# Kernel tuning notes

Measured on AMD Instinct MI355X. Metric: run time of the kernel, lower is better.

Reference implementation:

```python
import jax, jax.numpy as jnp
import numpy as np

POS_HALF = 4   # positive window: [t-4, t+4)
NEG_LEN = 12   # negatives: up to 12 frames on each side of the positive window
K_MAX = 2 * POS_HALF + 2 * NEG_LEN  # 32 candidates max per timestep


def _build_windows(T):
    """Static [T,K_MAX] gather indices + positive/valid masks (numpy, trace-time)."""
    idx = np.zeros((T, K_MAX), np.int32)
    pos_mask = np.zeros((T, K_MAX), bool)
    valid = np.zeros((T, K_MAX), bool)
    for t in range(T):
        start, end = max(0, t - POS_HALF), min(T, t + POS_HALF)
        pos = list(range(start, end))
        neg = list(range(max(0, start - NEG_LEN), start)) + \
              list(range(end, min(T, end + NEG_LEN)))
        comb = pos + neg
        idx[t, :len(comb)] = comb
        valid[t, :len(comb)] = True
        pos_mask[t, :len(pos)] = True
    return jnp.asarray(idx), jnp.asarray(pos_mask), jnp.asarray(valid)


def _directional(q, kv, idx, pos_mask, valid, scale, bias):
    # q, kv: [B,T,D] (L2-normalized); idx/pos_mask/valid: [T,K]
    w = kv[:, idx]  # [B,T,K,D] windowed gather
    logits = jnp.einsum('btd,btkd->btk', q, w) * scale + bias  # [B,T,K]
    sign = jnp.where(pos_mask, 1.0, -1.0)
    loglik = jax.nn.log_sigmoid(sign * logits)
    # per-t: sum over window, mean over batch; then sum over t
    loss = -jnp.where(valid, loglik, 0.0).sum(axis=2).mean(axis=0).sum()
    am = jnp.argmax(jnp.where(valid, logits, -jnp.inf), axis=2)  # [B,T]
    T = q.shape[1]
    correct = pos_mask[jnp.arange(T)[None, :], am].astype(jnp.float32).sum()
    return loss, correct


def setup_inputs() -> dict:
    key = jax.random.key(0)
    k1, k2 = jax.random.split(key)
    B, T, D = 8, 1024, 512
    return {
        "motion_feature": jax.random.normal(k1, (B, T, D), jnp.float32),
        "audio_feature": jax.random.normal(k2, (B, T, D), jnp.float32),
        "logit_scale": jnp.asarray(np.log(1.0 / 0.07), jnp.float32),  # param (pre-exp)
        "logit_bias": jnp.asarray(0.0, jnp.float32),                  # param
    }


def reference(motion_feature, audio_feature, logit_scale, logit_bias):
    B, T, _ = motion_feature.shape
    eps = 1e-12
    m = motion_feature / jnp.clip(
        jnp.linalg.norm(motion_feature, axis=2, keepdims=True), eps)
    a = audio_feature / jnp.clip(
        jnp.linalg.norm(audio_feature, axis=2, keepdims=True), eps)
    scale = jnp.exp(logit_scale)
    idx, pos_mask, valid = _build_windows(T)
    m2a_loss, m2a_correct = _directional(m, a, idx, pos_mask, valid, scale, logit_bias)
    a2m_loss, a2m_correct = _directional(a, m, idx, pos_mask, valid, scale, logit_bias)
    final_loss = (m2a_loss + a2m_loss) / (2 * T)
    total_correct = (m2a_correct + a2m_correct) / (2 * T * B)
    return final_loss, total_correct
```

## Files before the change

kernel.cpp:

```cpp
#include <hip/hip_runtime.h>
#include <math.h>

#define B_DIM 8
#define T_DIM 1024
#define D_DIM 512
#define BT (B_DIM * T_DIM)
#define NTILE 64
#define NBLK_BAND (B_DIM * NTILE)

typedef __bf16 bf16x8 __attribute__((ext_vector_type(8)));
typedef float floatx4 __attribute__((ext_vector_type(4)));

__device__ __forceinline__ float wave_reduce_sum(float v) {
#pragma unroll
    for (int off = 32; off > 0; off >>= 1) v += __shfl_xor(v, off, 64);
    return v;
}

__device__ __forceinline__ ushort f2bf(float x) {
    unsigned u = __float_as_uint(x);
    unsigned r = (u + 0x7fffu + ((u >> 16) & 1u)) >> 16;
    return (ushort)r;
}

__device__ __forceinline__ float softplus(float y) {
    return fmaxf(y, 0.0f) + log1pf(expf(-fabsf(y)));
}

__global__ __launch_bounds__(256) void prep_kernel(
    const float* __restrict__ m, const float* __restrict__ a,
    ushort* __restrict__ mhat, ushort* __restrict__ ahat)
{
    int wid  = blockIdx.x * 4 + (threadIdx.x >> 6);
    int lane = threadIdx.x & 63;
    const float4* mr = (const float4*)(m + (size_t)wid * D_DIM);
    const float4* ar = (const float4*)(a + (size_t)wid * D_DIM);
    float4 m0 = mr[lane], m1 = mr[lane + 64];
    float4 a0 = ar[lane], a1 = ar[lane + 64];
    float sm = m0.x*m0.x + m0.y*m0.y + m0.z*m0.z + m0.w*m0.w
             + m1.x*m1.x + m1.y*m1.y + m1.z*m1.z + m1.w*m1.w;
    float sa = a0.x*a0.x + a0.y*a0.y + a0.z*a0.z + a0.w*a0.w
             + a1.x*a1.x + a1.y*a1.y + a1.z*a1.z + a1.w*a1.w;
    sm = wave_reduce_sum(sm);
    sa = wave_reduce_sum(sa);
    float im = 1.0f / fmaxf(sqrtf(sm), 1e-12f);
    float ia = 1.0f / fmaxf(sqrtf(sa), 1e-12f);
    ushort4 mo0 = { f2bf(m0.x*im), f2bf(m0.y*im), f2bf(m0.z*im), f2bf(m0.w*im) };
    ushort4 mo1 = { f2bf(m1.x*im), f2bf(m1.y*im), f2bf(m1.z*im), f2bf(m1.w*im) };
    ushort4 ao0 = { f2bf(a0.x*ia), f2bf(a0.y*ia), f2bf(a0.z*ia), f2bf(a0.w*ia) };
    ushort4 ao1 = { f2bf(a1.x*ia), f2bf(a1.y*ia), f2bf(a1.z*ia), f2bf(a1.w*ia) };
    ushort4* mw = (ushort4*)(mhat + (size_t)wid * D_DIM);
    ushort4* aw = (ushort4*)(ahat + (size_t)wid * D_DIM);
    mw[lane] = mo0; mw[lane + 64] = mo1;
    aw[lane] = ao0; aw[lane + 64] = ao1;
}

__global__ __launch_bounds__(256) void bandloss_kernel(
    const ushort* __restrict__ mhat, const ushort* __restrict__ ahat,
    const float* __restrict__ pscale, const float* __restrict__ pbias,
    float2* __restrict__ pm,
    float* __restrict__ part_loss, float* __restrict__ part_corr)
{
    int blk = blockIdx.x;
    int b   = blk >> 6;
    int t0  = (blk & 63) << 4;
    int tid  = threadIdx.x;
    int w    = tid >> 6;
    int lane = tid & 63;
    int mrow = lane & 15;
    int kgrp = lane >> 4;

    const ushort* Abase = mhat + ((size_t)b << 19);
    const ushort* Bbase = ahat + ((size_t)b << 19);
    int koff = w * 128 + kgrp * 8;

    const ushort* arow = Abase + (size_t)(t0 + mrow) * D_DIM + koff;
    int j0 = max(t0 - 16 + mrow, 0);
    int j1 = t0 + mrow;
    int j2 = min(t0 + 16 + mrow, T_DIM - 1);
    const ushort* br0 = Bbase + (size_t)j0 * D_DIM + koff;
    const ushort* br1 = Bbase + (size_t)j1 * D_DIM + koff;
    const ushort* br2 = Bbase + (size_t)j2 * D_DIM + koff;

    floatx4 acc0 = {0.f,0.f,0.f,0.f};
    floatx4 acc1 = {0.f,0.f,0.f,0.f};
    floatx4 acc2 = {0.f,0.f,0.f,0.f};
#pragma unroll
    for (int ks = 0; ks < 4; ++ks) {
        bf16x8 af = *(const bf16x8*)(arow + ks * 32);
        bf16x8 b0 = *(const bf16x8*)(br0 + ks * 32);
        bf16x8 b1 = *(const bf16x8*)(br1 + ks * 32);
        bf16x8 b2 = *(const bf16x8*)(br2 + ks * 32);
        acc0 = __builtin_amdgcn_mfma_f32_16x16x32_bf16(af, b0, acc0, 0, 0, 0);
        acc1 = __builtin_amdgcn_mfma_f32_16x16x32_bf16(af, b1, acc1, 0, 0, 0);
        acc2 = __builtin_amdgcn_mfma_f32_16x16x32_bf16(af, b2, acc2, 0, 0, 0);
    }

    __shared__ float red[4][3][256];
#pragma unroll
    for (int r = 0; r < 4; ++r) {
        int rr = (kgrp * 4 + r) * 16 + mrow;
        red[w][0][rr] = acc0[r];
        red[w][1][rr] = acc1[r];
        red[w][2][rr] = acc2[r];
    }
    __syncthreads();

    int i  = tid >> 4;
    int cc = tid & 15;
    float s[3];
#pragma unroll
    for (int jt = 0; jt < 3; ++jt)
        s[jt] = red[0][jt][tid] + red[1][jt][tid]
              + red[2][jt][tid] + red[3][jt][tid];

    __shared__ float Sbuf[16][48];
#pragma unroll
    for (int jt = 0; jt < 3; ++jt)
        Sbuf[i][jt * 16 + cc] = s[jt];

    float scale = expf(pscale[0]), bias = pbias[0];
    float loss = 0.0f;
    float mmax = -1e30f, mpos = 0.0f;
#pragma unroll
    for (int jt = 0; jt < 3; ++jt) {
        int k  = jt * 16 + cc;
        int dd = k - i;
        int c  = t0 - 16 + k;
        bool cv = (c >= 0) && (c < T_DIM);
        if (cv && dd >= 0 && dd <= 32) {
            float logit = s[jt] * scale + bias;
            if (dd < 32) {
                bool pos = (dd >= 12) && (dd <= 19);
                loss += softplus(pos ? -logit : logit);
                if (s[jt] > mmax) { mmax = s[jt]; mpos = pos ? 1.0f : 0.0f; }
            }
            if (dd > 0) {
                bool pos = (dd >= 13) && (dd <= 20);
                loss += softplus(pos ? -logit : logit);
            }
        }
    }

#pragma unroll
    for (int off = 1; off < 16; off <<= 1) {
        float ov = __shfl_xor(mmax, off, 64);
        float op = __shfl_xor(mpos, off, 64);
        if (ov > mmax) { mmax = ov; mpos = op; }
    }
    __shared__ float rowpos[16];
    if (cc == 0) rowpos[i] = mpos;

    loss = wave_reduce_sum(loss);
    __shared__ float shl[4];
    if (lane == 0) shl[w] = loss;
    __syncthreads();

    if (tid < 48) {
        int k = tid;
        int c = t0 - 16 + k;
        float bv = -1e30f, bp = 0.0f;
        if (c >= 0 && c < T_DIM) {
            int ilo = max(0, k - 32), ihi = min(16, k);
            for (int ii = ilo; ii < ihi; ++ii) {
                float v = Sbuf[ii][k];
                if (v > bv) {
                    bv = v;
                    int dd = k - ii;
                    bp = (dd >= 13 && dd <= 20) ? 1.0f : 0.0f;
                }
            }
        }
        pm[blk * 48 + k] = make_float2(bv, bp);
    }
    if (tid == 0) {
        part_loss[blk] = shl[0] + shl[1] + shl[2] + shl[3];
        float cs = 0.0f;
        for (int r = 0; r < 16; ++r) cs += rowpos[r];
        part_corr[blk] = cs;
    }
}

__global__ __launch_bounds__(1024) void final2_kernel(
    const float2* __restrict__ pm,
    const float* __restrict__ part_loss, const float* __restrict__ part_corr,
    float* __restrict__ out)
{
    int tid = threadIdx.x;
    float corr = 0.0f, loss = 0.0f;

    for (int x = tid; x < BT; x += 1024) {
        int b = x >> 10, c = x & 1023;
        int tc = c >> 4;
        float bv = -1e30f, bp = 0.0f;
#pragma unroll
        for (int dp = -1; dp <= 1; ++dp) {
            int p = tc + dp;
            if (p < 0 || p >= NTILE) continue;
            int k = c - (p << 4) + 16;
            float2 v = pm[((b << 6) + p) * 48 + k];
            if (v.x > bv) { bv = v.x; bp = v.y; }
        }
        corr += bp;
    }
    if (tid < NBLK_BAND) {
        loss = part_loss[tid];
        corr += part_corr[tid];
    }

    loss = wave_reduce_sum(loss);
    corr = wave_reduce_sum(corr);
    __shared__ float shl[16], shc[16];
    int wv = tid >> 6, lane = tid & 63;
    if (lane == 0) { shl[wv] = loss; shc[wv] = corr; }
    __syncthreads();
    if (tid == 0) {
        float L = 0.0f, C = 0.0f;
#pragma unroll
        for (int r = 0; r < 16; ++r) { L += shl[r]; C += shc[r]; }
        out[0] = L / 16384.0f;
        out[1] = C / 16384.0f;
    }
}

extern "C" void kernel_launch(void* const* d_in, const int* in_sizes, int n_in,
                              void* d_out, int out_size, void* d_ws, size_t ws_size,
                              hipStream_t stream)
{
    const float* m  = (const float*)d_in[0];
    const float* a  = (const float*)d_in[1];
    const float* ps = (const float*)d_in[2];
    const float* pb = (const float*)d_in[3];
    float* out = (float*)d_out;

    const size_t MHAT_ELEMS = (size_t)BT * D_DIM;
    ushort* mhat = (ushort*)d_ws;
    ushort* ahat = mhat + MHAT_ELEMS;
    float2* pmb  = (float2*)(ahat + MHAT_ELEMS);
    float*  part_loss = (float*)(pmb + NBLK_BAND * 48);
    float*  part_corr = part_loss + NBLK_BAND;

    prep_kernel<<<BT / 4, 256, 0, stream>>>(m, a, mhat, ahat);
    bandloss_kernel<<<NBLK_BAND, 256, 0, stream>>>(mhat, ahat, ps, pb,
                                                   pmb, part_loss, part_corr);
    final2_kernel<<<1, 1024, 0, stream>>>(pmb, part_loss, part_corr, out);
}
```

Measured before the change: 100.8 us.

## Fuse normalization, band MFMA and final reduction into one kernel with atomics

Merges the three kernels into a single kernel. Each block loads its 16 query rows and 48 neighbor rows in fp32, L2-normalizes them, converts them to bf16 in shared memory, and runs the MFMA band products from LDS. Column argmax results are combined with packed-key atomicMax, loss and correct counts with atomicAdd, and the last block to finish does the final reduction. This removes the bf16 workspace round-trip and two launches. In exchange each neighbor row is read about three times across blocks, a memset is added, and the column argmax tie-breaking now depends on the packed key.

Result: slower. 126.1 us (+25.1%).

```diff
diff --git a/kernel.cpp b/kernel.cpp
--- a/kernel.cpp
+++ b/kernel.cpp
@@ -5,8 +5,8 @@
 #define T_DIM 1024
 #define D_DIM 512
 #define BT (B_DIM * T_DIM)
-#define NTILE 64
-#define NBLK_BAND (B_DIM * NTILE)
+#define NBLK 512
+#define LROW 520
 
 typedef __bf16 bf16x8 __attribute__((ext_vector_type(8)));
 typedef float floatx4 __attribute__((ext_vector_type(4)));
@@ -19,90 +19,106 @@
 
 __device__ __forceinline__ ushort f2bf(float x) {
     unsigned u = __float_as_uint(x);
-    unsigned r = (u + 0x7fffu + ((u >> 16) & 1u)) >> 16;
-    return (ushort)r;
+    return (ushort)((u + 0x7fffu + ((u >> 16) & 1u)) >> 16);
 }
 
 __device__ __forceinline__ float softplus(float y) {
     return fmaxf(y, 0.0f) + log1pf(expf(-fabsf(y)));
 }
 
-__global__ __launch_bounds__(256) void prep_kernel(
+__device__ __forceinline__ unsigned fkey(float f) {
+    unsigned u = __float_as_uint(f);
+    return (u & 0x80000000u) ? ~u : (u | 0x80000000u);
+}
+
+__global__ __launch_bounds__(256) void fused_kernel(
     const float* __restrict__ m, const float* __restrict__ a,
-    ushort* __restrict__ mhat, ushort* __restrict__ ahat)
+    const float* __restrict__ pscale, const float* __restrict__ pbias,
+    unsigned* __restrict__ colkey, float* __restrict__ gloss,
+    float* __restrict__ gcorr, unsigned* __restrict__ done,
+    float* __restrict__ out)
 {
-    int wid  = blockIdx.x * 4 + (threadIdx.x >> 6);
-    int lane = threadIdx.x & 63;
-    const float4* mr = (const float4*)(m + (size_t)wid * D_DIM);
-    const float4* ar = (const float4*)(a + (size_t)wid * D_DIM);
-    float4 m0 = mr[lane], m1 = mr[lane + 64];
-    float4 a0 = ar[lane], a1 = ar[lane + 64];
-    float sm = m0.x*m0.x + m0.y*m0.y + m0.z*m0.z + m0.w*m0.w
-             + m1.x*m1.x + m1.y*m1.y + m1.z*m1.z + m1.w*m1.w;
-    float sa = a0.x*a0.x + a0.y*a0.y + a0.z*a0.z + a0.w*a0.w
-             + a1.x*a1.x + a1.y*a1.y + a1.z*a1.z + a1.w*a1.w;
-    sm = wave_reduce_sum(sm);
-    sa = wave_reduce_sum(sa);
-    float im = 1.0f / fmaxf(sqrtf(sm), 1e-12f);
-    float ia = 1.0f / fmaxf(sqrtf(sa), 1e-12f);
-    ushort4 mo0 = { f2bf(m0.x*im), f2bf(m0.y*im), f2bf(m0.z*im), f2bf(m0.w*im) };
-    ushort4 mo1 = { f2bf(m1.x*im), f2bf(m1.y*im), f2bf(m1.z*im), f2bf(m1.w*im) };
-    ushort4 ao0 = { f2bf(a0.x*ia), f2bf(a0.y*ia), f2bf(a0.z*ia), f2bf(a0.w*ia) };
-    ushort4 ao1 = { f2bf(a1.x*ia), f2bf(a1.y*ia), f2bf(a1.z*ia), f2bf(a1.w*ia) };
-    ushort4* mw = (ushort4*)(mhat + (size_t)wid * D_DIM);
-    ushort4* aw = (ushort4*)(ahat + (size_t)wid * D_DIM);
-    mw[lane] = mo0; mw[lane + 64] = mo1;
-    aw[lane] = ao0; aw[lane + 64] = ao1;
-}
-
-__global__ __launch_bounds__(256) void bandloss_kernel(
-    const ushort* __restrict__ mhat, const ushort* __restrict__ ahat,
-    const float* __restrict__ pscale, const float* __restrict__ pbias,
-    float2* __restrict__ pm,
-    float* __restrict__ part_loss, float* __restrict__ part_corr)
-{
+    __shared__ char smraw[64 * LROW * 2];
+    ushort* stage  = (ushort*)smraw;
+    float*  red    = (float*)smraw;
+    float*  Sbuf   = (float*)(smraw + 12288);
+    float*  rowpos = (float*)(smraw + 15360);
+    float*  shl    = (float*)(smraw + 15424);
+    int*    lflag  = (int*)(smraw + 15440);
+
     int blk = blockIdx.x;
     int b   = blk >> 6;
     int t0  = (blk & 63) << 4;
     int tid  = threadIdx.x;
     int w    = tid >> 6;
     int lane = tid & 63;
-    int mrow = lane & 15;
-    int kgrp = lane >> 4;
-
-    const ushort* Abase = mhat + ((size_t)b << 19);
-    const ushort* Bbase = ahat + ((size_t)b << 19);
+
+    const float* mbase = m + ((size_t)b * T_DIM) * D_DIM;
+    const float* abase = a + ((size_t)b * T_DIM) * D_DIM;
+
+#pragma unroll
+    for (int i0 = 0; i0 < 16; i0 += 4) {
+        float4 da[4], db[4];
+        float ss[4];
+#pragma unroll
+        for (int r = 0; r < 4; ++r) {
+            int u = w * 16 + i0 + r;
+            const float4* p;
+            if (u < 16) {
+                p = (const float4*)(mbase + (size_t)(t0 + u) * D_DIM);
+            } else {
+                int gr = t0 - 16 + (u - 16);
+                gr = min(max(gr, 0), T_DIM - 1);
+                p = (const float4*)(abase + (size_t)gr * D_DIM);
+            }
+            da[r] = p[lane]; db[r] = p[lane + 64];
+            ss[r] = da[r].x*da[r].x + da[r].y*da[r].y + da[r].z*da[r].z + da[r].w*da[r].w
+                  + db[r].x*db[r].x + db[r].y*db[r].y + db[r].z*db[r].z + db[r].w*db[r].w;
+        }
+#pragma unroll
+        for (int off = 32; off > 0; off >>= 1) {
+#pragma unroll
+            for (int r = 0; r < 4; ++r) ss[r] += __shfl_xor(ss[r], off, 64);
+        }
+#pragma unroll
+        for (int r = 0; r < 4; ++r) {
+            int u = w * 16 + i0 + r;
+            float inv = 1.0f / fmaxf(sqrtf(ss[r]), 1e-12f);
+            ushort4 o0 = { f2bf(da[r].x*inv), f2bf(da[r].y*inv),
+                           f2bf(da[r].z*inv), f2bf(da[r].w*inv) };
+            ushort4 o1 = { f2bf(db[r].x*inv), f2bf(db[r].y*inv),
+                           f2bf(db[r].z*inv), f2bf(db[r].w*inv) };
+            *(ushort4*)&stage[u * LROW + lane * 4]       = o0;
+            *(ushort4*)&stage[u * LROW + 256 + lane * 4] = o1;
+        }
+    }
+    __syncthreads();
+
+    int mrow = lane & 15, kgrp = lane >> 4;
     int koff = w * 128 + kgrp * 8;
-
-    const ushort* arow = Abase + (size_t)(t0 + mrow) * D_DIM + koff;
-    int j0 = max(t0 - 16 + mrow, 0);
-    int j1 = t0 + mrow;
-    int j2 = min(t0 + 16 + mrow, T_DIM - 1);
-    const ushort* br0 = Bbase + (size_t)j0 * D_DIM + koff;
-    const ushort* br1 = Bbase + (size_t)j1 * D_DIM + koff;
-    const ushort* br2 = Bbase + (size_t)j2 * D_DIM + koff;
-
-    floatx4 acc0 = {0.f,0.f,0.f,0.f};
-    floatx4 acc1 = {0.f,0.f,0.f,0.f};
-    floatx4 acc2 = {0.f,0.f,0.f,0.f};
+    const ushort* Am = &stage[mrow * LROW + koff];
+    const ushort* B0 = &stage[(16 + mrow) * LROW + koff];
+    const ushort* B1 = &stage[(32 + mrow) * LROW + koff];
+    const ushort* B2 = &stage[(48 + mrow) * LROW + koff];
+    floatx4 acc0 = {0,0,0,0}, acc1 = {0,0,0,0}, acc2 = {0,0,0,0};
 #pragma unroll
     for (int ks = 0; ks < 4; ++ks) {
-        bf16x8 af = *(const bf16x8*)(arow + ks * 32);
-        bf16x8 b0 = *(const bf16x8*)(br0 + ks * 32);
-        bf16x8 b1 = *(const bf16x8*)(br1 + ks * 32);
-        bf16x8 b2 = *(const bf16x8*)(br2 + ks * 32);
-        acc0 = __builtin_amdgcn_mfma_f32_16x16x32_bf16(af, b0, acc0, 0, 0, 0);
-        acc1 = __builtin_amdgcn_mfma_f32_16x16x32_bf16(af, b1, acc1, 0, 0, 0);
-        acc2 = __builtin_amdgcn_mfma_f32_16x16x32_bf16(af, b2, acc2, 0, 0, 0);
-    }
-
-    __shared__ float red[4][3][256];
+        bf16x8 af = *(const bf16x8*)(Am + ks * 32);
+        bf16x8 f0 = *(const bf16x8*)(B0 + ks * 32);
+        bf16x8 f1 = *(const bf16x8*)(B1 + ks * 32);
+        bf16x8 f2 = *(const bf16x8*)(B2 + ks * 32);
+        acc0 = __builtin_amdgcn_mfma_f32_16x16x32_bf16(af, f0, acc0, 0, 0, 0);
+        acc1 = __builtin_amdgcn_mfma_f32_16x16x32_bf16(af, f1, acc1, 0, 0, 0);
+        acc2 = __builtin_amdgcn_mfma_f32_16x16x32_bf16(af, f2, acc2, 0, 0, 0);
+    }
+    __syncthreads();
+
 #pragma unroll
     for (int r = 0; r < 4; ++r) {
         int rr = (kgrp * 4 + r) * 16 + mrow;
-        red[w][0][rr] = acc0[r];
-        red[w][1][rr] = acc1[r];
-        red[w][2][rr] = acc2[r];
+        red[(w * 3 + 0) * 256 + rr] = acc0[r];
+        red[(w * 3 + 1) * 256 + rr] = acc1[r];
+        red[(w * 3 + 2) * 256 + rr] = acc2[r];
     }
     __syncthreads();
 
@@ -111,13 +127,11 @@
     float s[3];
 #pragma unroll
     for (int jt = 0; jt < 3; ++jt)
-        s[jt] = red[0][jt][tid] + red[1][jt][tid]
-              + red[2][jt][tid] + red[3][jt][tid];
-
-    __shared__ float Sbuf[16][48];
+        s[jt] = red[(0*3+jt)*256 + tid] + red[(1*3+jt)*256 + tid]
+              + red[(2*3+jt)*256 + tid] + red[(3*3+jt)*256 + tid];
 #pragma unroll
     for (int jt = 0; jt < 3; ++jt)
-        Sbuf[i][jt * 16 + cc] = s[jt];
+        Sbuf[i * 48 + jt * 16 + cc] = s[jt];
 
     float scale = expf(pscale[0]), bias = pbias[0];
     float loss = 0.0f;
@@ -148,78 +162,62 @@
         float op = __shfl_xor(mpos, off, 64);
         if (ov > mmax) { mmax = ov; mpos = op; }
     }
-    __shared__ float rowpos[16];
     if (cc == 0) rowpos[i] = mpos;
 
     loss = wave_reduce_sum(loss);
-    __shared__ float shl[4];
     if (lane == 0) shl[w] = loss;
     __syncthreads();
 
     if (tid < 48) {
         int k = tid;
         int c = t0 - 16 + k;
-        float bv = -1e30f, bp = 0.0f;
         if (c >= 0 && c < T_DIM) {
+            float bv = -1e30f; float bp = 0.0f;
             int ilo = max(0, k - 32), ihi = min(16, k);
             for (int ii = ilo; ii < ihi; ++ii) {
-                float v = Sbuf[ii][k];
+                float v = Sbuf[ii * 48 + k];
                 if (v > bv) {
                     bv = v;
                     int dd = k - ii;
                     bp = (dd >= 13 && dd <= 20) ? 1.0f : 0.0f;
                 }
             }
-        }
-        pm[blk * 48 + k] = make_float2(bv, bp);
+            unsigned key = (fkey(bv) & ~1u) | (bp > 0.5f ? 1u : 0u);
+            atomicMax(&colkey[(b << 10) + c], key);
+        }
     }
     if (tid == 0) {
-        part_loss[blk] = shl[0] + shl[1] + shl[2] + shl[3];
-        float cs = 0.0f;
-        for (int r = 0; r < 16; ++r) cs += rowpos[r];
-        part_corr[blk] = cs;
-    }
-}
-
-__global__ __launch_bounds__(1024) void final2_kernel(
-    const float2* __restrict__ pm,
-    const float* __restrict__ part_loss, const float* __restrict__ part_corr,
-    float* __restrict__ out)
-{
-    int tid = threadIdx.x;
-    float corr = 0.0f, loss = 0.0f;
-
-    for (int x = tid; x < BT; x += 1024) {
-        int b = x >> 10, c = x & 1023;
-        int tc = c >> 4;
-        float bv = -1e30f, bp = 0.0f;
-#pragma unroll
-        for (int dp = -1; dp <= 1; ++dp) {
-            int p = tc + dp;
-            if (p < 0 || p >= NTILE) continue;
-            int k = c - (p << 4) + 16;
-            float2 v = pm[((b << 6) + p) * 48 + k];
-            if (v.x > bv) { bv = v.x; bp = v.y; }
-        }
-        corr += bp;
-    }
-    if (tid < NBLK_BAND) {
-        loss = part_loss[tid];
-        corr += part_corr[tid];
-    }
-
-    loss = wave_reduce_sum(loss);
-    corr = wave_reduce_sum(corr);
-    __shared__ float shl[16], shc[16];
-    int wv = tid >> 6, lane = tid & 63;
-    if (lane == 0) { shl[wv] = loss; shc[wv] = corr; }
-    __syncthreads();
-    if (tid == 0) {
-        float L = 0.0f, C = 0.0f;
-#pragma unroll
-        for (int r = 0; r < 16; ++r) { L += shl[r]; C += shc[r]; }
-        out[0] = L / 16384.0f;
-        out[1] = C / 16384.0f;
+        float Lb = shl[0] + shl[1] + shl[2] + shl[3];
+        float Cb = 0.0f;
+        for (int r = 0; r < 16; ++r) Cb += rowpos[r];
+        atomicAdd(gloss, Lb);
+        atomicAdd(gcorr, Cb);
+    }
+
+    __threadfence();
+    __syncthreads();
+    if (tid == 0) lflag[0] = (atomicAdd(done, 1u) == (unsigned)(NBLK - 1)) ? 1 : 0;
+    __syncthreads();
+    if (lflag[0]) {
+        __threadfence();
+        float c2 = 0.0f;
+        for (int x = tid; x < BT; x += 256) {
+            unsigned k = __hip_atomic_load(&colkey[x], __ATOMIC_RELAXED,
+                                           __HIP_MEMORY_SCOPE_AGENT);
+            c2 += (float)(k & 1u);
+        }
+        c2 = wave_reduce_sum(c2);
+        if (lane == 0) shl[w] = c2;
+        __syncthreads();
+        if (tid == 0) {
+            float C2 = shl[0] + shl[1] + shl[2] + shl[3];
+            float L  = __hip_atomic_load(gloss, __ATOMIC_RELAXED,
+                                         __HIP_MEMORY_SCOPE_AGENT);
+            float C1 = __hip_atomic_load(gcorr, __ATOMIC_RELAXED,
+                                         __HIP_MEMORY_SCOPE_AGENT);
+            out[0] = L / 16384.0f;
+            out[1] = (C1 + C2) / 16384.0f;
+        }
     }
 }
 
@@ -233,15 +231,12 @@
     const float* pb = (const float*)d_in[3];
     float* out = (float*)d_out;
 
-    const size_t MHAT_ELEMS = (size_t)BT * D_DIM;
-    ushort* mhat = (ushort*)d_ws;
-    ushort* ahat = mhat + MHAT_ELEMS;
-    float2* pmb  = (float2*)(ahat + MHAT_ELEMS);
-    float*  part_loss = (float*)(pmb + NBLK_BAND * 48);
-    float*  part_corr = part_loss + NBLK_BAND;
-
-    prep_kernel<<<BT / 4, 256, 0, stream>>>(m, a, mhat, ahat);
-    bandloss_kernel<<<NBLK_BAND, 256, 0, stream>>>(mhat, ahat, ps, pb,
-                                                   pmb, part_loss, part_corr);
-    final2_kernel<<<1, 1024, 0, stream>>>(pmb, part_loss, part_corr, out);
-}
+    unsigned* colkey = (unsigned*)d_ws;
+    float*    gloss  = (float*)(colkey + BT);
+    float*    gcorr  = gloss + 1;
+    unsigned* done   = (unsigned*)(gcorr + 1);
+
+    hipMemsetAsync(d_ws, 0, (size_t)(BT + 3) * sizeof(unsigned), stream);
+    fused_kernel<<<NBLK, 256, 0, stream>>>(m, a, ps, pb,
+                                           colkey, gloss, gcorr, done, out);
+}
```

## Fuse final reduction into band kernel via atomics and last-block combine

Applied to the files above, without the earlier changes.

Removes the separate single-block final kernel. Column argmax is merged with atomicMax on order-preserving float keys that carry the positive flag in the low bit, and loss and correct counts are accumulated with atomicAdd. The last block to finish, detected through a done counter, reads the column keys and writes the outputs. Counters are zeroed inside the prep kernel. This saves one launch and the partial-buffer round trip, at the cost of atomic contention, a tail pass by one block, and argmax ties resolving on the flag bit instead of first index.

Measured after the change: 126.7 us. 25.7% more time.

```diff
diff --git a/kernel.cpp b/kernel.cpp
--- a/kernel.cpp
+++ b/kernel.cpp
@@ -5,8 +5,7 @@
 #define T_DIM 1024
 #define D_DIM 512
 #define BT (B_DIM * T_DIM)
-#define NTILE 64
-#define NBLK_BAND (B_DIM * NTILE)
+#define NBLK 512
 
 typedef __bf16 bf16x8 __attribute__((ext_vector_type(8)));
 typedef float floatx4 __attribute__((ext_vector_type(4)));
@@ -19,18 +18,29 @@
 
 __device__ __forceinline__ ushort f2bf(float x) {
     unsigned u = __float_as_uint(x);
-    unsigned r = (u + 0x7fffu + ((u >> 16) & 1u)) >> 16;
-    return (ushort)r;
+    return (ushort)((u + 0x7fffu + ((u >> 16) & 1u)) >> 16);
 }
 
 __device__ __forceinline__ float softplus(float y) {
     return fmaxf(y, 0.0f) + log1pf(expf(-fabsf(y)));
 }
 
+__device__ __forceinline__ unsigned fkey(float f) {
+    unsigned u = __float_as_uint(f);
+    return (u & 0x80000000u) ? ~u : (u | 0x80000000u);
+}
+
 __global__ __launch_bounds__(256) void prep_kernel(
     const float* __restrict__ m, const float* __restrict__ a,
-    ushort* __restrict__ mhat, ushort* __restrict__ ahat)
+    ushort* __restrict__ mhat, ushort* __restrict__ ahat,
+    unsigned* __restrict__ combine)
 {
+    if (blockIdx.x < 32) {
+        combine[(blockIdx.x << 8) + threadIdx.x] = 0u;
+    } else if (blockIdx.x == 32 && threadIdx.x < 3) {
+        combine[BT + threadIdx.x] = 0u;
+    }
+
     int wid  = blockIdx.x * 4 + (threadIdx.x >> 6);
     int lane = threadIdx.x & 63;
     const float4* mr = (const float4*)(m + (size_t)wid * D_DIM);
@@ -58,9 +68,16 @@
 __global__ __launch_bounds__(256) void bandloss_kernel(
     const ushort* __restrict__ mhat, const ushort* __restrict__ ahat,
     const float* __restrict__ pscale, const float* __restrict__ pbias,
-    float2* __restrict__ pm,
-    float* __restrict__ part_loss, float* __restrict__ part_corr)
+    unsigned* __restrict__ colkey, float* __restrict__ gloss,
+    float* __restrict__ gcorr, unsigned* __restrict__ done,
+    float* __restrict__ out)
 {
+    __shared__ float red[4][3][256];
+    __shared__ float Sbuf[16][48];
+    __shared__ float rowpos[16];
+    __shared__ float shl[4];
+    __shared__ int   lflag;
+
     int blk = blockIdx.x;
     int b   = blk >> 6;
     int t0  = (blk & 63) << 4;
@@ -82,21 +99,18 @@
     const ushort* br1 = Bbase + (size_t)j1 * D_DIM + koff;
     const ushort* br2 = Bbase + (size_t)j2 * D_DIM + koff;
 
-    floatx4 acc0 = {0.f,0.f,0.f,0.f};
-    floatx4 acc1 = {0.f,0.f,0.f,0.f};
-    floatx4 acc2 = {0.f,0.f,0.f,0.f};
+    floatx4 acc0 = {0,0,0,0}, acc1 = {0,0,0,0}, acc2 = {0,0,0,0};
 #pragma unroll
     for (int ks = 0; ks < 4; ++ks) {
         bf16x8 af = *(const bf16x8*)(arow + ks * 32);
-        bf16x8 b0 = *(const bf16x8*)(br0 + ks * 32);
-        bf16x8 b1 = *(const bf16x8*)(br1 + ks * 32);
-        bf16x8 b2 = *(const bf16x8*)(br2 + ks * 32);
-        acc0 = __builtin_amdgcn_mfma_f32_16x16x32_bf16(af, b0, acc0, 0, 0, 0);
-        acc1 = __builtin_amdgcn_mfma_f32_16x16x32_bf16(af, b1, acc1, 0, 0, 0);
-        acc2 = __builtin_amdgcn_mfma_f32_16x16x32_bf16(af, b2, acc2, 0, 0, 0);
-    }
-
-    __shared__ float red[4][3][256];
+        bf16x8 f0 = *(const bf16x8*)(br0 + ks * 32);
+        bf16x8 f1 = *(const bf16x8*)(br1 + ks * 32);
+        bf16x8 f2 = *(const bf16x8*)(br2 + ks * 32);
+        acc0 = __builtin_amdgcn_mfma_f32_16x16x32_bf16(af, f0, acc0, 0, 0, 0);
+        acc1 = __builtin_amdgcn_mfma_f32_16x16x32_bf16(af, f1, acc1, 0, 0, 0);
+        acc2 = __builtin_amdgcn_mfma_f32_16x16x32_bf16(af, f2, acc2, 0, 0, 0);
+    }
+
 #pragma unroll
     for (int r = 0; r < 4; ++r) {
         int rr = (kgrp * 4 + r) * 16 + mrow;
@@ -113,8 +127,6 @@
     for (int jt = 0; jt < 3; ++jt)
         s[jt] = red[0][jt][tid] + red[1][jt][tid]
               + red[2][jt][tid] + red[3][jt][tid];
-
-    __shared__ float Sbuf[16][48];
 #pragma unroll
     for (int jt = 0; jt < 3; ++jt)
         Sbuf[i][jt * 16 + cc] = s[jt];
@@ -148,19 +160,17 @@
         float op = __shfl_xor(mpos, off, 64);
         if (ov > mmax) { mmax = ov; mpos = op; }
     }
-    __shared__ float rowpos[16];
     if (cc == 0) rowpos[i] = mpos;
 
     loss = wave_reduce_sum(loss);
-    __shared__ float shl[4];
     if (lane == 0) shl[w] = loss;
     __syncthreads();
 
     if (tid < 48) {
         int k = tid;
         int c = t0 - 16 + k;
-        float bv = -1e30f, bp = 0.0f;
         if (c >= 0 && c < T_DIM) {
+            float bv = -1e30f; float bp = 0.0f;
             int ilo = max(0, k - 32), ihi = min(16, k);
             for (int ii = ilo; ii < ihi; ++ii) {
                 float v = Sbuf[ii][k];
@@ -170,56 +180,42 @@
                     bp = (dd >= 13 && dd <= 20) ? 1.0f : 0.0f;
                 }
             }
-        }
-        pm[blk * 48 + k] = make_float2(bv, bp);
+            unsigned key = (fkey(bv) & ~1u) | (bp > 0.5f ? 1u : 0u);
+            atomicMax(&colkey[(b << 10) + c], key);
+        }
     }
     if (tid == 0) {
-        part_loss[blk] = shl[0] + shl[1] + shl[2] + shl[3];
-        float cs = 0.0f;
-        for (int r = 0; r < 16; ++r) cs += rowpos[r];
-        part_corr[blk] = cs;
-    }
-}
-
-__global__ __launch_bounds__(1024) void final2_kernel(
-    const float2* __restrict__ pm,
-    const float* __restrict__ part_loss, const float* __restrict__ part_corr,
-    float* __restrict__ out)
-{
-    int tid = threadIdx.x;
-    float corr = 0.0f, loss = 0.0f;
-
-    for (int x = tid; x < BT; x += 1024) {
-        int b = x >> 10, c = x & 1023;
-        int tc = c >> 4;
-        float bv = -1e30f, bp = 0.0f;
-#pragma unroll
-        for (int dp = -1; dp <= 1; ++dp) {
-            int p = tc + dp;
-            if (p < 0 || p >= NTILE) continue;
-            int k = c - (p << 4) + 16;
-            float2 v = pm[((b << 6) + p) * 48 + k];
-            if (v.x > bv) { bv = v.x; bp = v.y; }
-        }
-        corr += bp;
-    }
-    if (tid < NBLK_BAND) {
-        loss = part_loss[tid];
-        corr += part_corr[tid];
-    }
-
-    loss = wave_reduce_sum(loss);
-    corr = wave_reduce_sum(corr);
-    __shared__ float shl[16], shc[16];
-    int wv = tid >> 6, lane = tid & 63;
-    if (lane == 0) { shl[wv] = loss; shc[wv] = corr; }
-    __syncthreads();
-    if (tid == 0) {
-        float L = 0.0f, C = 0.0f;
-#pragma unroll
-        for (int r = 0; r < 16; ++r) { L += shl[r]; C += shc[r]; }
-        out[0] = L / 16384.0f;
-        out[1] = C / 16384.0f;
+        float Lb = shl[0] + shl[1] + shl[2] + shl[3];
+        float Cb = 0.0f;
+        for (int r = 0; r < 16; ++r) Cb += rowpos[r];
+        atomicAdd(gloss, Lb);
+        atomicAdd(gcorr, Cb);
+    }
+
+    __threadfence();
+    __syncthreads();
+    if (tid == 0) lflag = (atomicAdd(done, 1u) == (unsigned)(NBLK - 1)) ? 1 : 0;
+    __syncthreads();
+    if (lflag) {
+        __threadfence();
+        float c2 = 0.0f;
+        for (int x = tid; x < BT; x += 256) {
+            unsigned k = __hip_atomic_load(&colkey[x], __ATOMIC_RELAXED,
+                                           __HIP_MEMORY_SCOPE_AGENT);
+            c2 += (float)(k & 1u);
+        }
+        c2 = wave_reduce_sum(c2);
+        if (lane == 0) shl[w] = c2;
+        __syncthreads();
+        if (tid == 0) {
+            float C2 = shl[0] + shl[1] + shl[2] + shl[3];
+            float L  = __hip_atomic_load(gloss, __ATOMIC_RELAXED,
+                                         __HIP_MEMORY_SCOPE_AGENT);
+            float C1 = __hip_atomic_load(gcorr, __ATOMIC_RELAXED,
+                                         __HIP_MEMORY_SCOPE_AGENT);
+            out[0] = L / 16384.0f;
+            out[1] = (C1 + C2) / 16384.0f;
+        }
     }
 }
 
@@ -236,12 +232,13 @@
     const size_t MHAT_ELEMS = (size_t)BT * D_DIM;
     ushort* mhat = (ushort*)d_ws;
     ushort* ahat = mhat + MHAT_ELEMS;
-    float2* pmb  = (float2*)(ahat + MHAT_ELEMS);
-    float*  part_loss = (float*)(pmb + NBLK_BAND * 48);
-    float*  part_corr = part_loss + NBLK_BAND;
-
-    prep_kernel<<<BT / 4, 256, 0, stream>>>(m, a, mhat, ahat);
-    bandloss_kernel<<<NBLK_BAND, 256, 0, stream>>>(mhat, ahat, ps, pb,
-                                                   pmb, part_loss, part_corr);
-    final2_kernel<<<1, 1024, 0, stream>>>(pmb, part_loss, part_corr, out);
-}
+    unsigned* combine = (unsigned*)(ahat + MHAT_ELEMS);
+    unsigned* colkey = combine;
+    float*    gloss  = (float*)(combine + BT);
+    float*    gcorr  = gloss + 1;
+    unsigned* done   = (unsigned*)(gcorr + 1);
+
+    prep_kernel<<<BT / 4, 256, 0, stream>>>(m, a, mhat, ahat, combine);
+    bandloss_kernel<<<NBLK, 256, 0, stream>>>(mhat, ahat, ps, pb,
+                                              colkey, gloss, gcorr, done, out);
+}
```

## Drop normalized bf16 intermediate; apply inverse norms after band MFMA

Applied to the files above, without the earlier changes.

The prep kernel no longer writes normalized bf16 copies of both feature tensors. It only computes per-row inverse L2 norms. The band kernel reads the raw fp32 features, converts them to bf16 in registers for the MFMA, and rescales the dot products by the row and column inverse norms afterward. This removes a full write and re-read of a bf16 intermediate, at the cost of the band kernel reading fp32 data (twice the bytes, with neighbouring rows read several times) and doing the conversion inline. It also changes rounding slightly, since unnormalized values are quantized to bf16.

Result: slower. 102.9 us (+2.1%).

```diff
diff --git a/kernel.cpp b/kernel.cpp
--- a/kernel.cpp
+++ b/kernel.cpp
@@ -6,7 +6,7 @@
 #define D_DIM 512
 #define BT (B_DIM * T_DIM)
 #define NTILE 64
-#define NBLK_BAND (B_DIM * NTILE)
+#define NBLK (B_DIM * NTILE)
 
 typedef __bf16 bf16x8 __attribute__((ext_vector_type(8)));
 typedef float floatx4 __attribute__((ext_vector_type(4)));
@@ -19,17 +19,25 @@
 
 __device__ __forceinline__ ushort f2bf(float x) {
     unsigned u = __float_as_uint(x);
-    unsigned r = (u + 0x7fffu + ((u >> 16) & 1u)) >> 16;
-    return (ushort)r;
+    return (ushort)((u + 0x7fffu + ((u >> 16) & 1u)) >> 16);
 }
 
 __device__ __forceinline__ float softplus(float y) {
     return fmaxf(y, 0.0f) + log1pf(expf(-fabsf(y)));
 }
 
-__global__ __launch_bounds__(256) void prep_kernel(
+__device__ __forceinline__ bf16x8 load_frag(const float* __restrict__ p) {
+    float4 x = *(const float4*)p;
+    float4 y = *(const float4*)(p + 4);
+    union { ushort u[8]; bf16x8 v; } r;
+    r.u[0] = f2bf(x.x); r.u[1] = f2bf(x.y); r.u[2] = f2bf(x.z); r.u[3] = f2bf(x.w);
+    r.u[4] = f2bf(y.x); r.u[5] = f2bf(y.y); r.u[6] = f2bf(y.z); r.u[7] = f2bf(y.w);
+    return r.v;
+}
+
+__global__ __launch_bounds__(256) void norm_kernel(
     const float* __restrict__ m, const float* __restrict__ a,
-    ushort* __restrict__ mhat, ushort* __restrict__ ahat)
+    float* __restrict__ invm, float* __restrict__ inva)
 {
     int wid  = blockIdx.x * 4 + (threadIdx.x >> 6);
     int lane = threadIdx.x & 63;
@@ -43,24 +51,24 @@
              + a1.x*a1.x + a1.y*a1.y + a1.z*a1.z + a1.w*a1.w;
     sm = wave_reduce_sum(sm);
     sa = wave_reduce_sum(sa);
-    float im = 1.0f / fmaxf(sqrtf(sm), 1e-12f);
-    float ia = 1.0f / fmaxf(sqrtf(sa), 1e-12f);
-    ushort4 mo0 = { f2bf(m0.x*im), f2bf(m0.y*im), f2bf(m0.z*im), f2bf(m0.w*im) };
-    ushort4 mo1 = { f2bf(m1.x*im), f2bf(m1.y*im), f2bf(m1.z*im), f2bf(m1.w*im) };
-    ushort4 ao0 = { f2bf(a0.x*ia), f2bf(a0.y*ia), f2bf(a0.z*ia), f2bf(a0.w*ia) };
-    ushort4 ao1 = { f2bf(a1.x*ia), f2bf(a1.y*ia), f2bf(a1.z*ia), f2bf(a1.w*ia) };
-    ushort4* mw = (ushort4*)(mhat + (size_t)wid * D_DIM);
-    ushort4* aw = (ushort4*)(ahat + (size_t)wid * D_DIM);
-    mw[lane] = mo0; mw[lane + 64] = mo1;
-    aw[lane] = ao0; aw[lane + 64] = ao1;
+    if (lane == 0) {
+        invm[wid] = 1.0f / fmaxf(sqrtf(sm), 1e-12f);
+        inva[wid] = 1.0f / fmaxf(sqrtf(sa), 1e-12f);
+    }
 }
 
 __global__ __launch_bounds__(256) void bandloss_kernel(
-    const ushort* __restrict__ mhat, const ushort* __restrict__ ahat,
+    const float* __restrict__ m, const float* __restrict__ a,
+    const float* __restrict__ invm, const float* __restrict__ inva,
     const float* __restrict__ pscale, const float* __restrict__ pbias,
     float2* __restrict__ pm,
     float* __restrict__ part_loss, float* __restrict__ part_corr)
 {
+    __shared__ float red[4][3][256];
+    __shared__ float Sbuf[16][48];
+    __shared__ float rowpos[16];
+    __shared__ float shl[4];
+
     int blk = blockIdx.x;
     int b   = blk >> 6;
     int t0  = (blk & 63) << 4;
@@ -70,33 +78,30 @@
     int mrow = lane & 15;
     int kgrp = lane >> 4;
 
-    const ushort* Abase = mhat + ((size_t)b << 19);
-    const ushort* Bbase = ahat + ((size_t)b << 19);
+    const float* mb = m + ((size_t)b << 19);
+    const float* ab = a + ((size_t)b << 19);
     int koff = w * 128 + kgrp * 8;
 
-    const ushort* arow = Abase + (size_t)(t0 + mrow) * D_DIM + koff;
+    const float* arow = mb + (size_t)(t0 + mrow) * D_DIM + koff;
     int j0 = max(t0 - 16 + mrow, 0);
     int j1 = t0 + mrow;
     int j2 = min(t0 + 16 + mrow, T_DIM - 1);
-    const ushort* br0 = Bbase + (size_t)j0 * D_DIM + koff;
-    const ushort* br1 = Bbase + (size_t)j1 * D_DIM + koff;
-    const ushort* br2 = Bbase + (size_t)j2 * D_DIM + koff;
-
-    floatx4 acc0 = {0.f,0.f,0.f,0.f};
-    floatx4 acc1 = {0.f,0.f,0.f,0.f};
-    floatx4 acc2 = {0.f,0.f,0.f,0.f};
+    const float* br0 = ab + (size_t)j0 * D_DIM + koff;
+    const float* br1 = ab + (size_t)j1 * D_DIM + koff;
+    const float* br2 = ab + (size_t)j2 * D_DIM + koff;
+
+    floatx4 acc0 = {0,0,0,0}, acc1 = {0,0,0,0}, acc2 = {0,0,0,0};
 #pragma unroll
     for (int ks = 0; ks < 4; ++ks) {
-        bf16x8 af = *(const bf16x8*)(arow + ks * 32);
-        bf16x8 b0 = *(const bf16x8*)(br0 + ks * 32);
-        bf16x8 b1 = *(const bf16x8*)(br1 + ks * 32);
-        bf16x8 b2 = *(const bf16x8*)(br2 + ks * 32);
-        acc0 = __builtin_amdgcn_mfma_f32_16x16x32_bf16(af, b0, acc0, 0, 0, 0);
-        acc1 = __builtin_amdgcn_mfma_f32_16x16x32_bf16(af, b1, acc1, 0, 0, 0);
-        acc2 = __builtin_amdgcn_mfma_f32_16x16x32_bf16(af, b2, acc2, 0, 0, 0);
-    }
-
-    __shared__ float red[4][3][256];
+        bf16x8 af = load_frag(arow + ks * 32);
+        bf16x8 f0 = load_frag(br0 + ks * 32);
+        bf16x8 f1 = load_frag(br1 + ks * 32);
+        bf16x8 f2 = load_frag(br2 + ks * 32);
+        acc0 = __builtin_amdgcn_mfma_f32_16x16x32_bf16(af, f0, acc0, 0, 0, 0);
+        acc1 = __builtin_amdgcn_mfma_f32_16x16x32_bf16(af, f1, acc1, 0, 0, 0);
+        acc2 = __builtin_amdgcn_mfma_f32_16x16x32_bf16(af, f2, acc2, 0, 0, 0);
+    }
+
 #pragma unroll
     for (int r = 0; r < 4; ++r) {
         int rr = (kgrp * 4 + r) * 16 + mrow;
@@ -113,13 +118,12 @@
     for (int jt = 0; jt < 3; ++jt)
         s[jt] = red[0][jt][tid] + red[1][jt][tid]
               + red[2][jt][tid] + red[3][jt][tid];
-
-    __shared__ float Sbuf[16][48];
 #pragma unroll
     for (int jt = 0; jt < 3; ++jt)
         Sbuf[i][jt * 16 + cc] = s[jt];
 
     float scale = expf(pscale[0]), bias = pbias[0];
+    float im_i  = invm[(b << 10) + t0 + i];
     float loss = 0.0f;
     float mmax = -1e30f, mpos = 0.0f;
 #pragma unroll
@@ -129,11 +133,13 @@
         int c  = t0 - 16 + k;
         bool cv = (c >= 0) && (c < T_DIM);
         if (cv && dd >= 0 && dd <= 32) {
-            float logit = s[jt] * scale + bias;
+            float ia_c  = inva[(b << 10) + c];
+            float sv    = s[jt] * ia_c;
+            float logit = sv * im_i * scale + bias;
             if (dd < 32) {
                 bool pos = (dd >= 12) && (dd <= 19);
                 loss += softplus(pos ? -logit : logit);
-                if (s[jt] > mmax) { mmax = s[jt]; mpos = pos ? 1.0f : 0.0f; }
+                if (sv > mmax) { mmax = sv; mpos = pos ? 1.0f : 0.0f; }
             }
             if (dd > 0) {
                 bool pos = (dd >= 13) && (dd <= 20);
@@ -148,11 +154,9 @@
         float op = __shfl_xor(mpos, off, 64);
         if (ov > mmax) { mmax = ov; mpos = op; }
     }
-    __shared__ float rowpos[16];
     if (cc == 0) rowpos[i] = mpos;
 
     loss = wave_reduce_sum(loss);
-    __shared__ float shl[4];
     if (lane == 0) shl[w] = loss;
     __syncthreads();
 
@@ -163,7 +167,7 @@
         if (c >= 0 && c < T_DIM) {
             int ilo = max(0, k - 32), ihi = min(16, k);
             for (int ii = ilo; ii < ihi; ++ii) {
-                float v = Sbuf[ii][k];
+                float v = Sbuf[ii][k] * invm[(b << 10) + t0 + ii];
                 if (v > bv) {
                     bv = v;
                     int dd = k - ii;
@@ -174,9 +178,9 @@
         pm[blk * 48 + k] = make_float2(bv, bp);
     }
     if (tid == 0) {
-        part_loss[blk] = shl[0] + shl[1] + shl[2] + shl[3];
         float cs = 0.0f;
         for (int r = 0; r < 16; ++r) cs += rowpos[r];
+        part_loss[blk] = shl[0] + shl[1] + shl[2] + shl[3];
         part_corr[blk] = cs;
     }
 }
@@ -203,7 +207,7 @@
         }
         corr += bp;
     }
-    if (tid < NBLK_BAND) {
+    if (tid < NBLK) {
         loss = part_loss[tid];
         corr += part_corr[tid];
     }
@@ -233,15 +237,15 @@
     const float* pb = (const float*)d_in[3];
     float* out = (float*)d_out;
 
-    const size_t MHAT_ELEMS = (size_t)BT * D_DIM;
-    ushort* mhat = (ushort*)d_ws;
-    ushort* ahat = mhat + MHAT_ELEMS;
-    float2* pmb  = (float2*)(ahat + MHAT_ELEMS);
-    float*  part_loss = (float*)(pmb + NBLK_BAND * 48);
-    float*  part_corr = part_loss + NBLK_BAND;
-
-    prep_kernel<<<BT / 4, 256, 0, stream>>>(m, a, mhat, ahat);
-    bandloss_kernel<<<NBLK_BAND, 256, 0, stream>>>(mhat, ahat, ps, pb,
-                                                   pmb, part_loss, part_corr);
-    final2_kernel<<<1, 1024, 0, stream>>>(pmb, part_loss, part_corr, out);
-}
+    float*  ws        = (float*)d_ws;
+    float*  invm      = ws;
+    float*  inva      = ws + BT;
+    float2* pm        = (float2*)(ws + 2 * BT);
+    float*  part_loss = (float*)(pm + NBLK * 48);
+    float*  part_corr = part_loss + NBLK;
+
+    norm_kernel<<<BT / 4, 256, 0, stream>>>(m, a, invm, inva);
+    bandloss_kernel<<<NBLK, 256, 0, stream>>>(m, a, invm, inva, ps, pb,
+                                              pm, part_loss, part_corr);
+    final2_kernel<<<1, 1024, 0, stream>>>(pm, part_loss, part_corr, out);
+}
```
